# Kernel tuning notes

Measured on AMD Instinct MI355X. Metric: run time of the kernel, lower is better.

Reference implementation:

```python
import jax, jax.numpy as jnp
import numpy as np

B, C, H, W = 16, 5, 768, 768  # num_classes = 5 (labels 0..4 per the remapping logic)


def setup_inputs() -> dict:
    key = jax.random.key(0)
    k1, k2 = jax.random.split(key)
    pred = jax.random.normal(k1, (B, C, H, W), dtype=jnp.float32)
    gt = jax.random.randint(k2, (B, H, W), 0, 5, dtype=jnp.int32)
    return {"pred": pred, "gt": gt, "negative_ratio": 3}


def reference(pred, gt, negative_ratio):
    num_classes = pred.shape[1]
    # [B,C,H,W] -> [B,H,W,C] -> [N,C]
    predict = jnp.transpose(pred, (0, 2, 3, 1)).reshape(-1, num_classes)
    target = gt.reshape(-1)

    # label remap 4->0, 2->1, 3->1 defines the pos/neg split (original labels kept for CE)
    pos = (target == 1) | (target == 2) | (target == 3)
    neg = ~pos

    # per-pixel cross entropy vs ORIGINAL labels
    logp = jax.nn.log_softmax(predict, axis=-1)            # [N, C]
    ce = -jnp.take_along_axis(logp, target[:, None].astype(jnp.int32), axis=-1)[:, 0]  # [N]

    n_pos = jnp.sum(pos).astype(jnp.int32)
    # int(negative_ratio * n_pos) truncates toward zero in torch; floor == trunc for non-negative
    n_neg = jnp.minimum(jnp.sum(neg).astype(jnp.int32),
                        (negative_ratio * n_pos.astype(jnp.float32)).astype(jnp.int32))

    loss_pos = jnp.sum(jnp.where(pos, ce, 0.0))

    # hard-negative mining: top-n_neg of negative CE (dynamic k via sort + prefix mask)
    neg_ce = jnp.where(neg, ce, -jnp.inf)
    sorted_desc = jnp.sort(neg_ce)[::-1]
    idx = jnp.arange(sorted_desc.shape[0], dtype=jnp.int32)
    loss_neg = jnp.sum(jnp.where(idx < n_neg, sorted_desc, 0.0))

    return (loss_pos + loss_neg) / (n_pos + n_neg).astype(pred.dtype)
```

## Files before the change

kernel.cpp:

```cpp
#include <hip/hip_runtime.h>


static constexpr int B_ = 16, C_ = 5, H_ = 768, W_ = 768;
static constexpr int HW_ = H_ * W_;
static constexpr int NPIX_ = B_ * HW_;
static constexpr int PIX_PER_BLK_ = 4096;
static constexpr int NBLK_ = NPIX_ / PIX_PER_BLK_;
static constexpr int BLKS_PER_B_ = HW_ / PIX_PER_BLK_;

struct Slot { float lp; float lall; unsigned cp; unsigned pad; };

__device__ __forceinline__ unsigned f2ord(float f) {
    unsigned u = __float_as_uint(f);
    return (u & 0x80000000u) ? ~u : (u | 0x80000000u);
}
__device__ __forceinline__ float ord2f(unsigned o) {
    unsigned v = (o & 0x80000000u) ? (o & 0x7FFFFFFFu) : ~o;
    return __uint_as_float(v);
}

__device__ __forceinline__ float pixel_ce_precise(const float* __restrict__ pred, int p, int t) {
    const int b = p / HW_;
    const int hw = p - b * HW_;
    const float* base = pred + (size_t)b * (C_ * HW_) + hw;
    const float x0 = base[0], x1 = base[HW_], x2 = base[2 * HW_],
                x3 = base[3 * HW_], x4 = base[4 * HW_];
    const float m = fmaxf(fmaxf(fmaxf(x0, x1), fmaxf(x2, x3)), x4);
    const float lse = m + logf(expf(x0 - m) + expf(x1 - m) + expf(x2 - m) +
                               expf(x3 - m) + expf(x4 - m));
    const float xt = (t == 0) ? x0 : (t == 1) ? x1 : (t == 2) ? x2 : (t == 3) ? x3 : x4;
    return lse - xt;
}

__global__ __launch_bounds__(256, 4) void k_ce_pass(const float* __restrict__ pred,
                                                    const int* __restrict__ gt,
                                                    Slot* __restrict__ slots) {
    const int bb = blockIdx.x / BLKS_PER_B_;
    const int hw0 = (blockIdx.x - bb * BLKS_PER_B_) * PIX_PER_BLK_ + threadIdx.x * 4;
    const float* base = pred + (size_t)bb * (C_ * HW_) + hw0;
    const int* gbase = gt + bb * HW_ + hw0;

    float4 v[4][5];
    int4 t4[4];
#pragma unroll
    for (int c = 0; c < 4; ++c) {
        const float* cb = base + c * 1024;
#pragma unroll
        for (int pl = 0; pl < 5; ++pl)
            v[c][pl] = *reinterpret_cast<const float4*>(cb + pl * HW_);
        t4[c] = *reinterpret_cast<const int4*>(gbase + c * 1024);
    }

    float lp = 0.f, lall = 0.f;
    unsigned cp = 0u;

    auto pix = [&](float x0, float x1, float x2, float x3, float x4, int t) {
        const float se = __expf(x0) + __expf(x1) + __expf(x2) + __expf(x3) + __expf(x4);
        const float xt = (t == 0) ? x0 : (t == 1) ? x1 : (t == 2) ? x2 : (t == 3) ? x3 : x4;
        const float ce = __logf(se) - xt;
        const bool pos = ((unsigned)(t - 1) <= 2u);
        lall += ce;
        lp += pos ? ce : 0.0f;
        cp += pos ? 1u : 0u;
    };
#pragma unroll
    for (int c = 0; c < 4; ++c) {
        pix(v[c][0].x, v[c][1].x, v[c][2].x, v[c][3].x, v[c][4].x, t4[c].x);
        pix(v[c][0].y, v[c][1].y, v[c][2].y, v[c][3].y, v[c][4].y, t4[c].y);
        pix(v[c][0].z, v[c][1].z, v[c][2].z, v[c][3].z, v[c][4].z, t4[c].z);
        pix(v[c][0].w, v[c][1].w, v[c][2].w, v[c][3].w, v[c][4].w, t4[c].w);
    }

#pragma unroll
    for (int off = 32; off > 0; off >>= 1) {
        lp += __shfl_down(lp, off);
        lall += __shfl_down(lall, off);
        cp += __shfl_down(cp, off);
    }
    __shared__ float s_lp[4], s_la[4];
    __shared__ unsigned s_cp[4];
    const int wid = threadIdx.x >> 6;
    const int lane = threadIdx.x & 63;
    if (lane == 0) { s_lp[wid] = lp; s_la[wid] = lall; s_cp[wid] = cp; }
    __syncthreads();
    if (threadIdx.x == 0) {
        Slot s;
        s.lp = s_lp[0] + s_lp[1] + s_lp[2] + s_lp[3];
        s.lall = s_la[0] + s_la[1] + s_la[2] + s_la[3];
        s.cp = s_cp[0] + s_cp[1] + s_cp[2] + s_cp[3];
        s.pad = 0u;
        slots[blockIdx.x] = s;
    }
}

__global__ __launch_bounds__(256) void k_finalize(const float* __restrict__ pred,
                                                  const int* __restrict__ gt,
                                                  const int* __restrict__ ratio,
                                                  const Slot* __restrict__ slots,
                                                  float* __restrict__ out) {
    double dlp = 0.0, dla = 0.0;
    unsigned c = 0u;
#pragma unroll
    for (int i = 0; i < NBLK_ / 256; ++i) {
        const Slot s = slots[i * 256 + threadIdx.x];
        dlp += (double)s.lp;
        dla += (double)s.lall;
        c += s.cp;
    }
#pragma unroll
    for (int off = 32; off > 0; off >>= 1) {
        dlp += __shfl_down(dlp, off);
        dla += __shfl_down(dla, off);
        c += __shfl_down(c, off);
    }
    __shared__ double sdp[4], sda[4];
    __shared__ unsigned sc[4];
    __shared__ double t_lp, t_la;
    __shared__ unsigned t_cp;
    {
        const int wid = threadIdx.x >> 6;
        const int lane = threadIdx.x & 63;
        if (lane == 0) { sdp[wid] = dlp; sda[wid] = dla; sc[wid] = c; }
        __syncthreads();
        if (threadIdx.x == 0) {
            t_lp = sdp[0] + sdp[1] + sdp[2] + sdp[3];
            t_la = sda[0] + sda[1] + sda[2] + sda[3];
            t_cp = sc[0] + sc[1] + sc[2] + sc[3];
        }
        __syncthreads();
    }
    const double loss_pos = t_lp;
    const double sum_neg = t_la - t_lp;
    const unsigned cp = t_cp;
    const unsigned cn = (unsigned)NPIX_ - cp;

    const float rf = (float)ratio[0];
    long long nneg_ll = (long long)(rf * (float)cp);
    if (nneg_ll < 0) nneg_ll = 0;
    const unsigned nneg = (unsigned)((nneg_ll < (long long)cn) ? nneg_ll : (long long)cn);
    const double denom = (double)cp + (double)nneg;

    if (nneg >= cn) {
        if (threadIdx.x == 0)
            out[0] = (denom > 0.0) ? (float)((loss_pos + sum_neg) / denom) : 0.0f;
        return;
    }
    if (nneg == 0) {
        if (threadIdx.x == 0)
            out[0] = (denom > 0.0) ? (float)(loss_pos / denom) : 0.0f;
        return;
    }

    __shared__ unsigned s_hist[256];
    __shared__ unsigned s_prefix, s_k;
    if (threadIdx.x == 0) { s_prefix = 0u; s_k = nneg; }
    __syncthreads();
    for (int round = 0; round < 4; ++round) {
        const int shift = 24 - 8 * round;
        for (int i = threadIdx.x; i < 256; i += blockDim.x) s_hist[i] = 0u;
        __syncthreads();
        const unsigned prefix = s_prefix;
        const unsigned pmask = (round == 0) ? 0u : (0xFFFFFFFFu << (shift + 8));
        for (int p = threadIdx.x; p < NPIX_; p += blockDim.x) {
            const int t = gt[p];
            if ((unsigned)(t - 1) <= 2u) continue;
            const unsigned key = f2ord(pixel_ce_precise(pred, p, t));
            if ((key & pmask) == prefix)
                atomicAdd(&s_hist[(key >> shift) & 255u], 1u);
        }
        __syncthreads();
        if (threadIdx.x == 0) {
            const unsigned kk = s_k;
            unsigned cum = 0u;
            for (int i = 255; i >= 0; --i) {
                const unsigned h = s_hist[i];
                if (cum + h >= kk) {
                    s_k = kk - cum;
                    s_prefix = prefix | ((unsigned)i << shift);
                    break;
                }
                cum += h;
            }
        }
        __syncthreads();
    }
    const unsigned Tkey = s_prefix;
    const float Tval = ord2f(Tkey);
    double sgt = 0.0;
    unsigned cgt = 0u;
    for (int p = threadIdx.x; p < NPIX_; p += blockDim.x) {
        const int t = gt[p];
        if ((unsigned)(t - 1) <= 2u) continue;
        const float ce = pixel_ce_precise(pred, p, t);
        if (f2ord(ce) > Tkey) { sgt += (double)ce; ++cgt; }
    }
#pragma unroll
    for (int off = 32; off > 0; off >>= 1) {
        sgt += __shfl_down(sgt, off);
        cgt += __shfl_down(cgt, off);
    }
    __shared__ double s_s[4];
    __shared__ unsigned s_c[4];
    const int wid = threadIdx.x >> 6;
    const int lane = threadIdx.x & 63;
    if (lane == 0) { s_s[wid] = sgt; s_c[wid] = cgt; }
    __syncthreads();
    if (threadIdx.x == 0) {
        double S = 0.0;
        unsigned Cg = 0u;
        for (int w = 0; w < 4; ++w) { S += s_s[w]; Cg += s_c[w]; }
        const double loss_neg = S + (double)(nneg - Cg) * (double)Tval;
        out[0] = (float)((loss_pos + loss_neg) / denom);
    }
}

extern "C" void kernel_launch(void* const* d_in, const int* in_sizes, int n_in,
                              void* d_out, int out_size, void* d_ws, size_t ws_size,
                              hipStream_t stream) {
    const float* pred = (const float*)d_in[0];
    const int* gt = (const int*)d_in[1];
    const int* ratio = (const int*)d_in[2];
    float* out = (float*)d_out;
    Slot* slots = (Slot*)d_ws;

    k_ce_pass<<<NBLK_, 256, 0, stream>>>(pred, gt, slots);
    k_finalize<<<1, 256, 0, stream>>>(pred, gt, ratio, slots, out);
}
```

Measured before the change: 43.31 us.

## Fuse CE pass and finalize into one kernel with flag-based completion

Merges the per-block cross-entropy reduction and the finalize kernel into a single launch. Each block publishes its partial sums with a release-store of a magic flag, and block 0 spin-waits with acquire loads until every slot is flagged before finishing the reduction. The grid also shrinks from 2304 to 768 blocks, each handling three 4096-pixel groups. The aim is to drop the second launch and the gap between kernels. The flags are never reset, so on repeated calls block 0 can read stale slots from an earlier run, and block 0 spinning relies on all blocks becoming resident.

```diff
diff --git a/kernel.cpp b/kernel.cpp
--- a/kernel.cpp
+++ b/kernel.cpp
@@ -4,11 +4,13 @@
 static constexpr int B_ = 16, C_ = 5, H_ = 768, W_ = 768;
 static constexpr int HW_ = H_ * W_;
 static constexpr int NPIX_ = B_ * HW_;
-static constexpr int PIX_PER_BLK_ = 4096;
-static constexpr int NBLK_ = NPIX_ / PIX_PER_BLK_;
-static constexpr int BLKS_PER_B_ = HW_ / PIX_PER_BLK_;
-
-struct Slot { float lp; float lall; unsigned cp; unsigned pad; };
+static constexpr int NBLK_ = 768;
+static constexpr int BLKS_PER_B_ = NBLK_ / B_;
+static constexpr int PIX_PER_BLK_ = HW_ / BLKS_PER_B_;
+static constexpr int GROUPS_ = 3;
+static constexpr unsigned MAGIC_ = 0x5ca1ab1eu;
+
+struct Slot { float lp; float lall; unsigned cp; unsigned flag; };
 
 __device__ __forceinline__ unsigned f2ord(float f) {
     unsigned u = __float_as_uint(f);
@@ -32,43 +34,49 @@
     return lse - xt;
 }
 
-__global__ __launch_bounds__(256, 4) void k_ce_pass(const float* __restrict__ pred,
-                                                    const int* __restrict__ gt,
-                                                    Slot* __restrict__ slots) {
+__global__ __launch_bounds__(256, 4) void k_fused(const float* __restrict__ pred,
+                                                  const int* __restrict__ gt,
+                                                  const int* __restrict__ ratio,
+                                                  Slot* __restrict__ slots,
+                                                  float* __restrict__ out) {
     const int bb = blockIdx.x / BLKS_PER_B_;
-    const int hw0 = (blockIdx.x - bb * BLKS_PER_B_) * PIX_PER_BLK_ + threadIdx.x * 4;
-    const float* base = pred + (size_t)bb * (C_ * HW_) + hw0;
-    const int* gbase = gt + bb * HW_ + hw0;
-
-    float4 v[4][5];
-    int4 t4[4];
-#pragma unroll
-    for (int c = 0; c < 4; ++c) {
-        const float* cb = base + c * 1024;
-#pragma unroll
-        for (int pl = 0; pl < 5; ++pl)
-            v[c][pl] = *reinterpret_cast<const float4*>(cb + pl * HW_);
-        t4[c] = *reinterpret_cast<const int4*>(gbase + c * 1024);
-    }
+    const int hwB = (blockIdx.x - bb * BLKS_PER_B_) * PIX_PER_BLK_;
+    const float* base = pred + (size_t)bb * (C_ * HW_) + hwB + threadIdx.x * 4;
+    const int* gbase = gt + bb * HW_ + hwB + threadIdx.x * 4;
 
     float lp = 0.f, lall = 0.f;
     unsigned cp = 0u;
 
-    auto pix = [&](float x0, float x1, float x2, float x3, float x4, int t) {
-        const float se = __expf(x0) + __expf(x1) + __expf(x2) + __expf(x3) + __expf(x4);
-        const float xt = (t == 0) ? x0 : (t == 1) ? x1 : (t == 2) ? x2 : (t == 3) ? x3 : x4;
-        const float ce = __logf(se) - xt;
-        const bool pos = ((unsigned)(t - 1) <= 2u);
-        lall += ce;
-        lp += pos ? ce : 0.0f;
-        cp += pos ? 1u : 0u;
-    };
-#pragma unroll
-    for (int c = 0; c < 4; ++c) {
-        pix(v[c][0].x, v[c][1].x, v[c][2].x, v[c][3].x, v[c][4].x, t4[c].x);
-        pix(v[c][0].y, v[c][1].y, v[c][2].y, v[c][3].y, v[c][4].y, t4[c].y);
-        pix(v[c][0].z, v[c][1].z, v[c][2].z, v[c][3].z, v[c][4].z, t4[c].z);
-        pix(v[c][0].w, v[c][1].w, v[c][2].w, v[c][3].w, v[c][4].w, t4[c].w);
+#pragma unroll
+    for (int g = 0; g < GROUPS_; ++g) {
+        const int off = g * 4096;
+        float4 v[4][5];
+        int4 t4[4];
+#pragma unroll
+        for (int c = 0; c < 4; ++c) {
+            const float* cb = base + off + c * 1024;
+#pragma unroll
+            for (int pl = 0; pl < 5; ++pl)
+                v[c][pl] = *reinterpret_cast<const float4*>(cb + pl * HW_);
+            t4[c] = *reinterpret_cast<const int4*>(gbase + off + c * 1024);
+        }
+        auto pix = [&](float x0, float x1, float x2, float x3, float x4, int t) {
+            const float se = __expf(x0) + __expf(x1) + __expf(x2) + __expf(x3) + __expf(x4);
+            const float xt = (t == 0) ? x0 : (t == 1) ? x1 : (t == 2) ? x2
+                           : (t == 3) ? x3 : x4;
+            const float ce = __logf(se) - xt;
+            const bool pos = ((unsigned)(t - 1) <= 2u);
+            lall += ce;
+            lp += pos ? ce : 0.0f;
+            cp += pos ? 1u : 0u;
+        };
+#pragma unroll
+        for (int c = 0; c < 4; ++c) {
+            pix(v[c][0].x, v[c][1].x, v[c][2].x, v[c][3].x, v[c][4].x, t4[c].x);
+            pix(v[c][0].y, v[c][1].y, v[c][2].y, v[c][3].y, v[c][4].y, t4[c].y);
+            pix(v[c][0].z, v[c][1].z, v[c][2].z, v[c][3].z, v[c][4].z, t4[c].z);
+            pix(v[c][0].w, v[c][1].w, v[c][2].w, v[c][3].w, v[c][4].w, t4[c].w);
+        }
     }
 
 #pragma unroll
@@ -79,33 +87,32 @@
     }
     __shared__ float s_lp[4], s_la[4];
     __shared__ unsigned s_cp[4];
-    const int wid = threadIdx.x >> 6;
-    const int lane = threadIdx.x & 63;
-    if (lane == 0) { s_lp[wid] = lp; s_la[wid] = lall; s_cp[wid] = cp; }
-    __syncthreads();
-    if (threadIdx.x == 0) {
-        Slot s;
-        s.lp = s_lp[0] + s_lp[1] + s_lp[2] + s_lp[3];
-        s.lall = s_la[0] + s_la[1] + s_la[2] + s_la[3];
-        s.cp = s_cp[0] + s_cp[1] + s_cp[2] + s_cp[3];
-        s.pad = 0u;
-        slots[blockIdx.x] = s;
-    }
-}
-
-__global__ __launch_bounds__(256) void k_finalize(const float* __restrict__ pred,
-                                                  const int* __restrict__ gt,
-                                                  const int* __restrict__ ratio,
-                                                  const Slot* __restrict__ slots,
-                                                  float* __restrict__ out) {
+    {
+        const int wid = threadIdx.x >> 6;
+        const int lane = threadIdx.x & 63;
+        if (lane == 0) { s_lp[wid] = lp; s_la[wid] = lall; s_cp[wid] = cp; }
+        __syncthreads();
+        if (threadIdx.x == 0) {
+            Slot* s = &slots[blockIdx.x];
+            s->lp = s_lp[0] + s_lp[1] + s_lp[2] + s_lp[3];
+            s->lall = s_la[0] + s_la[1] + s_la[2] + s_la[3];
+            s->cp = s_cp[0] + s_cp[1] + s_cp[2] + s_cp[3];
+            __hip_atomic_store(&s->flag, MAGIC_, __ATOMIC_RELEASE,
+                               __HIP_MEMORY_SCOPE_AGENT);
+        }
+    }
+    if (blockIdx.x != 0) return;
+
     double dlp = 0.0, dla = 0.0;
     unsigned c = 0u;
 #pragma unroll
     for (int i = 0; i < NBLK_ / 256; ++i) {
-        const Slot s = slots[i * 256 + threadIdx.x];
-        dlp += (double)s.lp;
-        dla += (double)s.lall;
-        c += s.cp;
+        Slot* s = &slots[i * 256 + threadIdx.x];
+        while (__hip_atomic_load(&s->flag, __ATOMIC_ACQUIRE,
+                                 __HIP_MEMORY_SCOPE_AGENT) != MAGIC_) {}
+        dlp += (double)s->lp;
+        dla += (double)s->lall;
+        c += s->cp;
     }
 #pragma unroll
     for (int off = 32; off > 0; off >>= 1) {
@@ -131,14 +138,14 @@
     }
     const double loss_pos = t_lp;
     const double sum_neg = t_la - t_lp;
-    const unsigned cp = t_cp;
-    const unsigned cn = (unsigned)NPIX_ - cp;
+    const unsigned cpx = t_cp;
+    const unsigned cn = (unsigned)NPIX_ - cpx;
 
     const float rf = (float)ratio[0];
-    long long nneg_ll = (long long)(rf * (float)cp);
+    long long nneg_ll = (long long)(rf * (float)cpx);
     if (nneg_ll < 0) nneg_ll = 0;
     const unsigned nneg = (unsigned)((nneg_ll < (long long)cn) ? nneg_ll : (long long)cn);
-    const double denom = (double)cp + (double)nneg;
+    const double denom = (double)cpx + (double)nneg;
 
     if (nneg >= cn) {
         if (threadIdx.x == 0)
@@ -201,16 +208,18 @@
     }
     __shared__ double s_s[4];
     __shared__ unsigned s_c[4];
-    const int wid = threadIdx.x >> 6;
-    const int lane = threadIdx.x & 63;
-    if (lane == 0) { s_s[wid] = sgt; s_c[wid] = cgt; }
-    __syncthreads();
-    if (threadIdx.x == 0) {
-        double S = 0.0;
-        unsigned Cg = 0u;
-        for (int w = 0; w < 4; ++w) { S += s_s[w]; Cg += s_c[w]; }
-        const double loss_neg = S + (double)(nneg - Cg) * (double)Tval;
-        out[0] = (float)((loss_pos + loss_neg) / denom);
+    {
+        const int wid = threadIdx.x >> 6;
+        const int lane = threadIdx.x & 63;
+        if (lane == 0) { s_s[wid] = sgt; s_c[wid] = cgt; }
+        __syncthreads();
+        if (threadIdx.x == 0) {
+            double S = 0.0;
+            unsigned Cg = 0u;
+            for (int w = 0; w < 4; ++w) { S += s_s[w]; Cg += s_c[w]; }
+            const double loss_neg = S + (double)(nneg - Cg) * (double)Tval;
+            out[0] = (float)((loss_pos + loss_neg) / denom);
+        }
     }
 }
 
@@ -223,6 +232,5 @@
     float* out = (float*)d_out;
     Slot* slots = (Slot*)d_ws;
 
-    k_ce_pass<<<NBLK_, 256, 0, stream>>>(pred, gt, slots);
-    k_finalize<<<1, 256, 0, stream>>>(pred, gt, ratio, slots, out);
-}
+    k_fused<<<NBLK_, 256, 0, stream>>>(pred, gt, ratio, slots, out);
+}
```

Measured after the change: 159.1 us. 267% more time.
